# Performance work log

Hardware: AMD Instinct MI355X
Metric: run time of the kernel (lower is better)

The kernel has to match this reference:

```python
import jax, jax.numpy as jnp
import numpy as np

D_MODEL = 1024
N_EXPERTS = 8
TOP_K = 2
FFN_HIDDEN = 4 * D_MODEL


def setup_inputs() -> dict:
    key = jax.random.key(0)
    ks = jax.random.split(key, 6)
    # xavier-uniform-ish scales
    def xavier(k, shape):
        fan_in, fan_out = shape[-2], shape[-1]
        lim = jnp.sqrt(6.0 / (fan_in + fan_out))
        return jax.random.uniform(k, shape, jnp.float32, -lim, lim)
    x = jax.random.normal(ks[0], (4, 2048, D_MODEL), jnp.float32)
    w_gate = xavier(ks[1], (N_EXPERTS, D_MODEL))
    W1 = xavier(ks[2], (N_EXPERTS, D_MODEL, FFN_HIDDEN))
    b1 = jnp.zeros((N_EXPERTS, FFN_HIDDEN), jnp.float32)
    W2 = xavier(ks[3], (N_EXPERTS, FFN_HIDDEN, D_MODEL))
    b2 = jnp.zeros((N_EXPERTS, D_MODEL), jnp.float32)
    return {"x": x, "w_gate": w_gate, "W1": W1, "b1": b1, "W2": W2, "b2": b2}


def reference(x, w_gate, W1, b1, W2, b2):
    B, S, D = x.shape
    flat_x = x.reshape(-1, D)  # [T, D]
    gate = jax.nn.softmax(flat_x @ w_gate.T, axis=-1)  # [T, E]
    topk_scores, topk_idx = jax.lax.top_k(gate, TOP_K)  # [T, K]
    # combine weights per (token, expert); topk indices are distinct per token
    cw = (jax.nn.one_hot(topk_idx, N_EXPERTS, dtype=flat_x.dtype)
          * topk_scores[..., None]).sum(axis=1)  # [T, E]
    # all-expert FFN (dense grouped GEMM), then weighted combine
    h = jax.nn.gelu(jnp.einsum('td,edh->teh', flat_x, W1) + b1, approximate=False)
    y = jnp.einsum('teh,ehd->ted', h, W2) + b2  # [T, E, D]
    out = jnp.einsum('ted,te->td', y, cw)
    return out.reshape(B, S, D)
```

## Files before the change

kernel.cpp:

```cpp
#include <hip/hip_runtime.h>
#include <hip/hip_bf16.h>
#include <math.h>

#define TTOK 8192
#define DM   1024
#define NE   8
#define FH   4096
#define ECAP 8192

typedef __attribute__((ext_vector_type(8))) short bf16x8;
typedef __attribute__((ext_vector_type(4))) float f32x4;

__device__ __forceinline__ unsigned short f2bf(float f) {
  union { float f; unsigned u; } v; v.f = f;
  unsigned r = v.u + 0x7fffu + ((v.u >> 16) & 1u);
  return (unsigned short)(r >> 16);
}

__device__ __forceinline__ void async16(const unsigned short* g, unsigned short* l) {
  __builtin_amdgcn_global_load_lds(
      (const __attribute__((address_space(1))) void*)g,
      (__attribute__((address_space(3))) void*)l, 16, 0, 0);
}

__device__ __forceinline__ float gelu_erf(float v) {
  float x = v * 0.70710678118654752f;
  float ax = fabsf(x);
  float t = __frcp_rn(1.0f + 0.3275911f * ax);
  float poly = t * (0.254829592f + t * (-0.284496736f +
               t * (1.421413741f + t * (-1.453152027f + t * 1.061405429f))));
  float erfa = 1.0f - poly * __expf(-ax * ax);
  float erfx = copysignf(erfa, x);
  return 0.5f * v * (1.0f + erfx);
}

__global__ void cvt_x(const float* __restrict__ x, unsigned short* __restrict__ xb, int n4) {
  int id = blockIdx.x * 256 + threadIdx.x;
  if (id >= n4) return;
  float4 v = ((const float4*)x)[id];
  ushort4 o;
  o.x = f2bf(v.x); o.y = f2bf(v.y); o.z = f2bf(v.z); o.w = f2bf(v.w);
  ((ushort4*)xb)[id] = o;
}

__global__ __launch_bounds__(256) void transpose_cvt(
    const float* __restrict__ src, unsigned short* __restrict__ dst, int R, int Cc) {
  __shared__ unsigned short t[64 * 72];
  int e = blockIdx.z;
  int c0 = blockIdx.x * 64, r0 = blockIdx.y * 64;
  int tid = threadIdx.x;
  const float* sp = src + (size_t)e * R * Cc;
  unsigned short* dp = dst + (size_t)e * R * Cc;
#pragma unroll
  for (int p = 0; p < 4; ++p) {
    int idx = p * 256 + tid;
    int row = idx >> 4;
    int c4 = (idx & 15) * 4;
    float4 v = *(const float4*)(sp + (size_t)(r0 + row) * Cc + c0 + c4);
    t[(c4 + 0) * 72 + row] = f2bf(v.x);
    t[(c4 + 1) * 72 + row] = f2bf(v.y);
    t[(c4 + 2) * 72 + row] = f2bf(v.z);
    t[(c4 + 3) * 72 + row] = f2bf(v.w);
  }
  __syncthreads();
#pragma unroll
  for (int p = 0; p < 4; ++p) {
    int idx = p * 256 + tid;
    int crow = idx >> 4;
    int r4 = (idx & 15) * 4;
    ushort4 o = *(ushort4*)(&t[crow * 72 + r4]);
    *(ushort4*)(dp + (size_t)(c0 + crow) * R + r0 + r4) = o;
  }
}

__global__ __launch_bounds__(256) void gate_kernel(
    const float* __restrict__ x, const float* __restrict__ wg,
    int* __restrict__ cnt, int* __restrict__ ent_tok, float* __restrict__ ent_w) {
  __shared__ float wls[NE * DM];
  int tid = threadIdx.x;
  for (int i = tid; i < NE * DM / 4; i += 256)
    ((float4*)wls)[i] = ((const float4*)wg)[i];
  __syncthreads();

  int wave = tid >> 6, lane = tid & 63;
  int t = blockIdx.x * 4 + wave;
  const float* xp = x + (size_t)t * DM;
  float acc[NE];
#pragma unroll
  for (int e = 0; e < NE; ++e) acc[e] = 0.f;
#pragma unroll
  for (int i = 0; i < 16; ++i) {
    float xv = xp[i * 64 + lane];
#pragma unroll
    for (int e = 0; e < NE; ++e) acc[e] += xv * wls[e * DM + i * 64 + lane];
  }
#pragma unroll
  for (int e = 0; e < NE; ++e) {
    float v = acc[e];
    for (int off = 32; off; off >>= 1) v += __shfl_xor(v, off, 64);
    acc[e] = v;
  }
  if (lane == 0) {
    float mx = acc[0];
#pragma unroll
    for (int e = 1; e < NE; ++e) mx = fmaxf(mx, acc[e]);
    float p[NE], s = 0.f;
#pragma unroll
    for (int e = 0; e < NE; ++e) { p[e] = __expf(acc[e] - mx); s += p[e]; }
    float inv = 1.f / s;
#pragma unroll
    for (int e = 0; e < NE; ++e) p[e] *= inv;
    int i0 = 0; float m0v = p[0];
#pragma unroll
    for (int e = 1; e < NE; ++e) if (p[e] > m0v) { m0v = p[e]; i0 = e; }
    int i1 = -1; float m1v = -1.f;
#pragma unroll
    for (int e = 0; e < NE; ++e) if (e != i0 && p[e] > m1v) { m1v = p[e]; i1 = e; }
    int pos0 = atomicAdd(&cnt[i0], 1);
    ent_tok[i0 * ECAP + pos0] = t * 2;
    ent_w[i0 * ECAP + pos0] = m0v;
    int pos1 = atomicAdd(&cnt[i1], 1);
    ent_tok[i1 * ECAP + pos1] = t * 2 + 1;
    ent_w[i1 * ECAP + pos1] = m1v;
  }
}

__global__ void scan_cnt(const int* __restrict__ cnt, int* __restrict__ base) {
  if (threadIdx.x == 0) {
    int s = 0;
    for (int e = 0; e < NE; ++e) { base[e] = s; s += cnt[e]; }
  }
}

#define ISSUE_A(buf, k0)                                         \
  async16(asrc0 + (k0), &As[buf][tid * 8]);                      \
  async16(asrc1 + (k0), &As[buf][2048 + tid * 8]);

#define COMPUTE(buf)                                                           \
  {                                                                            \
    bf16x8 af[4], bfr[4];                                                      \
    _Pragma("unroll") for (int im = 0; im < 4; ++im)                           \
      af[im] = *(const bf16x8*)(&As[buf][(wm * 64 + im * 16 + l16) * 32 + q * 8]); \
    _Pragma("unroll") for (int in = 0; in < 4; ++in)                           \
      bfr[in] = *(const bf16x8*)(&Bs[buf][(wn * 64 + in * 16 + l16) * 32 + q * 8]); \
    _Pragma("unroll") for (int im = 0; im < 4; ++im)                           \
      _Pragma("unroll") for (int in = 0; in < 4; ++in)                         \
        acc[im][in] = __builtin_amdgcn_mfma_f32_16x16x32_bf16(af[im], bfr[in], acc[im][in], 0, 0, 0); \
  }

__global__ __launch_bounds__(256) void moe_gemm1(
    const unsigned short* __restrict__ xb, const unsigned short* __restrict__ W1T,
    const float* __restrict__ b1, const int* __restrict__ cnt,
    const int* __restrict__ base, const int* __restrict__ ent_tok,
    unsigned short* __restrict__ hbuf) {
  const int bid = blockIdx.x;
  const int e = bid & 7;
  const int j = bid >> 3;
  const int n0 = (j >> 6) * 128;
  const int m0 = (j & 63) * 128;
  const int C = cnt[e];
  if (m0 >= C) return;
  const int be = base[e];
  const int tid = threadIdx.x;
  const int lane = tid & 63, wave = tid >> 6;
  const int wm = wave & 1, wn = wave >> 1;
  const int q = lane >> 4, l16 = lane & 15;

  __shared__ unsigned short As[2][128 * 32];
  __shared__ unsigned short Bs[2][128 * 32];
  __shared__ float bls[128];

  if (tid < 128) bls[tid] = b1[e * FH + n0 + tid];

  const int r = tid >> 2;
  const int kq = (tid & 3) * 8;
  int i0 = m0 + r;      if (i0 >= C) i0 = C - 1;
  int i1 = m0 + r + 64; if (i1 >= C) i1 = C - 1;
  const unsigned short* asrc0 = xb + (size_t)(ent_tok[e * ECAP + i0] >> 1) * DM + kq;
  const unsigned short* asrc1 = xb + (size_t)(ent_tok[e * ECAP + i1] >> 1) * DM + kq;
  const unsigned short* bsrc  = W1T + ((size_t)e * FH + n0 + r) * DM + kq;

  f32x4 acc[4][4];
#pragma unroll
  for (int i = 0; i < 4; ++i)
#pragma unroll
    for (int jj = 0; jj < 4; ++jj) acc[i][jj] = (f32x4){0.f, 0.f, 0.f, 0.f};

  ISSUE_A(0, 0)
  async16(bsrc, &Bs[0][tid * 8]);
  async16(bsrc + (size_t)64 * DM, &Bs[0][2048 + tid * 8]);

#pragma unroll 1
  for (int k0 = 0; k0 < DM; k0 += 64) {
    __syncthreads();
    if (k0 + 32 < DM) {
      ISSUE_A(1, k0 + 32)
      async16(bsrc + k0 + 32, &Bs[1][tid * 8]);
      async16(bsrc + (size_t)64 * DM + k0 + 32, &Bs[1][2048 + tid * 8]);
    }
    COMPUTE(0)
    __syncthreads();
    if (k0 + 64 < DM) {
      ISSUE_A(0, k0 + 64)
      async16(bsrc + k0 + 64, &Bs[0][tid * 8]);
      async16(bsrc + (size_t)64 * DM + k0 + 64, &Bs[0][2048 + tid * 8]);
    }
    COMPUTE(1)
  }

#pragma unroll
  for (int im = 0; im < 4; ++im)
#pragma unroll
    for (int rr = 0; rr < 4; ++rr) {
      int gm = m0 + wm * 64 + im * 16 + q * 4 + rr;
      if (gm >= C) continue;
      size_t bas = (size_t)(be + gm) * FH;
#pragma unroll
      for (int in = 0; in < 4; ++in) {
        int n = wn * 64 + in * 16 + l16;
        float v = acc[im][in][rr] + bls[n];
        hbuf[bas + n0 + n] = f2bf(gelu_erf(v));
      }
    }
}

__global__ __launch_bounds__(256) void moe_gemm2(
    const unsigned short* __restrict__ hbuf, const unsigned short* __restrict__ W2T,
    const float* __restrict__ b2, const int* __restrict__ cnt,
    const int* __restrict__ base, const int* __restrict__ ent_tok,
    const float* __restrict__ ent_w, float* __restrict__ ybuf) {
  const int bid = blockIdx.x;
  const int e = bid & 7;
  const int j = bid >> 3;
  const int n0 = (j >> 6) * 128;
  const int m0 = (j & 63) * 128;
  const int C = cnt[e];
  if (m0 >= C) return;
  const int be = base[e];
  const int tid = threadIdx.x;
  const int lane = tid & 63, wave = tid >> 6;
  const int wm = wave & 1, wn = wave >> 1;
  const int q = lane >> 4, l16 = lane & 15;

  __shared__ unsigned short As[2][128 * 32];
  __shared__ unsigned short Bs[2][128 * 32];
  __shared__ float bls[128];

  if (tid < 128) bls[tid] = b2[e * DM + n0 + tid];

  const int r = tid >> 2;
  const int kq = (tid & 3) * 8;
  int i0 = m0 + r;      if (i0 >= C) i0 = C - 1;
  int i1 = m0 + r + 64; if (i1 >= C) i1 = C - 1;
  const unsigned short* asrc0 = hbuf + (size_t)(be + i0) * FH + kq;
  const unsigned short* asrc1 = hbuf + (size_t)(be + i1) * FH + kq;
  const unsigned short* bsrc  = W2T + ((size_t)e * DM + n0 + r) * FH + kq;

  f32x4 acc[4][4];
#pragma unroll
  for (int i = 0; i < 4; ++i)
#pragma unroll
    for (int jj = 0; jj < 4; ++jj) acc[i][jj] = (f32x4){0.f, 0.f, 0.f, 0.f};

  ISSUE_A(0, 0)
  async16(bsrc, &Bs[0][tid * 8]);
  async16(bsrc + (size_t)64 * FH, &Bs[0][2048 + tid * 8]);

#pragma unroll 1
  for (int k0 = 0; k0 < FH; k0 += 64) {
    __syncthreads();
    if (k0 + 32 < FH) {
      ISSUE_A(1, k0 + 32)
      async16(bsrc + k0 + 32, &Bs[1][tid * 8]);
      async16(bsrc + (size_t)64 * FH + k0 + 32, &Bs[1][2048 + tid * 8]);
    }
    COMPUTE(0)
    __syncthreads();
    if (k0 + 64 < FH) {
      ISSUE_A(0, k0 + 64)
      async16(bsrc + k0 + 64, &Bs[0][tid * 8]);
      async16(bsrc + (size_t)64 * FH + k0 + 64, &Bs[0][2048 + tid * 8]);
    }
    COMPUTE(1)
  }

#pragma unroll
  for (int im = 0; im < 4; ++im)
#pragma unroll
    for (int rr = 0; rr < 4; ++rr) {
      int gm = m0 + wm * 64 + im * 16 + q * 4 + rr;
      if (gm >= C) continue;
      int rowid = ent_tok[e * ECAP + gm];
      float w = ent_w[e * ECAP + gm];
      size_t bas = (size_t)rowid * DM;
#pragma unroll
      for (int in = 0; in < 4; ++in) {
        int n = wn * 64 + in * 16 + l16;
        ybuf[bas + n0 + n] = w * (acc[im][in][rr] + bls[n]);
      }
    }
}

__global__ void combine_k(const float* __restrict__ y, float* __restrict__ out, int n4) {
  int id = blockIdx.x * 256 + threadIdx.x;
  if (id >= n4) return;
  int t = id >> 8;
  int c = id & 255;
  float4 a = ((const float4*)y)[((size_t)t * 2) * 256 + c];
  float4 b = ((const float4*)y)[((size_t)t * 2 + 1) * 256 + c];
  float4 o = {a.x + b.x, a.y + b.y, a.z + b.z, a.w + b.w};
  ((float4*)out)[id] = o;
}

extern "C" void kernel_launch(void* const* d_in, const int* in_sizes, int n_in,
                              void* d_out, int out_size, void* d_ws, size_t ws_size,
                              hipStream_t stream) {
  const float* x  = (const float*)d_in[0];
  const float* wg = (const float*)d_in[1];
  const float* W1 = (const float*)d_in[2];
  const float* b1 = (const float*)d_in[3];
  const float* W2 = (const float*)d_in[4];
  const float* b2 = (const float*)d_in[5];
  float* out = (float*)d_out;

  char* ws = (char*)d_ws;
  size_t off = 0;
  unsigned short* xb = (unsigned short*)(ws + off); off += (size_t)TTOK * DM * 2;
  int* cnt = (int*)(ws + off); off += 128;
  int* base = (int*)(ws + off); off += 128;
  int* ent_tok = (int*)(ws + off); off += (size_t)NE * ECAP * 4;
  float* ent_w = (float*)(ws + off); off += (size_t)NE * ECAP * 4;
  unsigned short* W1T = (unsigned short*)(ws + off); off += (size_t)NE * DM * FH * 2;
  unsigned short* W2T = (unsigned short*)(ws + off); off += (size_t)NE * FH * DM * 2;
  unsigned short* hbuf = (unsigned short*)(ws + off); off += (size_t)TTOK * 2 * FH * 2;
  float* ybuf = (float*)W1T;

  hipMemsetAsync(cnt, 0, 128, stream);
  cvt_x<<<TTOK * DM / 4 / 256, 256, 0, stream>>>(x, xb, TTOK * DM / 4);
  gate_kernel<<<TTOK / 4, 256, 0, stream>>>(x, wg, cnt, ent_tok, ent_w);
  scan_cnt<<<1, 64, 0, stream>>>(cnt, base);
  dim3 t1(FH / 64, DM / 64, NE);
  transpose_cvt<<<t1, 256, 0, stream>>>(W1, W1T, DM, FH);
  dim3 t2(DM / 64, FH / 64, NE);
  transpose_cvt<<<t2, 256, 0, stream>>>(W2, W2T, FH, DM);
  moe_gemm1<<<16384, 256, 0, stream>>>(xb, W1T, b1, cnt, base, ent_tok, hbuf);
  moe_gemm2<<<4096, 256, 0, stream>>>(hbuf, W2T, b2, cnt, base, ent_tok, ent_w, ybuf);
  combine_k<<<TTOK * DM / 4 / 256, 256, 0, stream>>>(ybuf, out, TTOK * DM / 4);
}
```

Before: 1.027 ms.

## Replace MoE grouped GEMMs with 256x256 tile, 8-wave, swizzled LDS pipelined kernel

```diff
diff --git a/kernel.cpp b/kernel.cpp
--- a/kernel.cpp
+++ b/kernel.cpp
@@ -132,171 +132,162 @@
   }
 }
 
-#define ISSUE_A(buf, k0)                                         \
-  async16(asrc0 + (k0), &As[buf][tid * 8]);                      \
-  async16(asrc1 + (k0), &As[buf][2048 + tid * 8]);
-
-#define COMPUTE(buf)                                                           \
-  {                                                                            \
-    bf16x8 af[4], bfr[4];                                                      \
-    _Pragma("unroll") for (int im = 0; im < 4; ++im)                           \
-      af[im] = *(const bf16x8*)(&As[buf][(wm * 64 + im * 16 + l16) * 32 + q * 8]); \
-    _Pragma("unroll") for (int in = 0; in < 4; ++in)                           \
-      bfr[in] = *(const bf16x8*)(&Bs[buf][(wn * 64 + in * 16 + l16) * 32 + q * 8]); \
-    _Pragma("unroll") for (int im = 0; im < 4; ++im)                           \
-      _Pragma("unroll") for (int in = 0; in < 4; ++in)                         \
-        acc[im][in] = __builtin_amdgcn_mfma_f32_16x16x32_bf16(af[im], bfr[in], acc[im][in], 0, 0, 0); \
-  }
-
-__global__ __launch_bounds__(256) void moe_gemm1(
-    const unsigned short* __restrict__ xb, const unsigned short* __restrict__ W1T,
-    const float* __restrict__ b1, const int* __restrict__ cnt,
+
+#define LDS_BAR __builtin_amdgcn_s_barrier()
+#define WAITLGKM asm volatile("s_waitcnt lgkmcnt(0)" ::: "memory")
+#define WAITVM4  asm volatile("s_waitcnt vmcnt(4)" ::: "memory")
+#define WAITVM0  asm volatile("s_waitcnt vmcnt(0)" ::: "memory")
+
+#define LD_A8(imb)                                                                \
+  _Pragma("unroll") for (int ii = 0; ii < 4; ++ii) {                              \
+    af[ii][0] = *(const bf16x8*)(aBase + ((imb) + ii) * 2048 + rowbA + colb0);    \
+    af[ii][1] = *(const bf16x8*)(aBase + ((imb) + ii) * 2048 + rowbA + colb1);    \
+  }
+
+#define LD_B4(inb)                                                                \
+  _Pragma("unroll") for (int jj = 0; jj < 2; ++jj) {                              \
+    bf[(inb) + jj][0] = *(const bf16x8*)(bBase + ((inb) + jj) * 2048 + rowbB + colb0); \
+    bf[(inb) + jj][1] = *(const bf16x8*)(bBase + ((inb) + jj) * 2048 + rowbB + colb1); \
+  }
+
+#define MMAQ(imb, inb)                                                            \
+  _Pragma("unroll") for (int ii = 0; ii < 4; ++ii)                                \
+  _Pragma("unroll") for (int jj = 0; jj < 2; ++jj) {                              \
+    acc[(imb) + ii][(inb) + jj] = __builtin_amdgcn_mfma_f32_16x16x32_bf16(        \
+        af[ii][0], bf[(inb) + jj][0], acc[(imb) + ii][(inb) + jj], 0, 0, 0);      \
+    acc[(imb) + ii][(inb) + jj] = __builtin_amdgcn_mfma_f32_16x16x32_bf16(        \
+        af[ii][1], bf[(inb) + jj][1], acc[(imb) + ii][(inb) + jj], 0, 0, 0);      \
+  }
+
+#define STG_A(b, h, k0) {                                                         \
+    async16(pA[(h) * 2 + 0] + (k0), &sA[(b)][(h)][tid * 8]);                      \
+    async16(pA[(h) * 2 + 1] + (k0), &sA[(b)][(h)][4096 + tid * 8]);               \
+  }
+#define STG_B(b, h, k0) {                                                         \
+    async16(pB[(h) * 2 + 0] + (k0), &sB[(b)][(h)][tid * 8]);                      \
+    async16(pB[(h) * 2 + 1] + (k0), &sB[(b)][(h)][4096 + tid * 8]);               \
+  }
+
+template <int KTOT, int NTOT, bool GELU>
+__global__ __launch_bounds__(512, 2) void moe_gemm8(
+    const unsigned short* __restrict__ Asrc, const unsigned short* __restrict__ Bsrc,
+    const float* __restrict__ bias, const int* __restrict__ cnt,
     const int* __restrict__ base, const int* __restrict__ ent_tok,
-    unsigned short* __restrict__ hbuf) {
+    const float* __restrict__ ent_w, unsigned short* __restrict__ hout,
+    float* __restrict__ yout) {
   const int bid = blockIdx.x;
   const int e = bid & 7;
   const int j = bid >> 3;
-  const int n0 = (j >> 6) * 128;
-  const int m0 = (j & 63) * 128;
+  const int mt = j & 31;
+  const int nt = j >> 5;
   const int C = cnt[e];
+  const int m0 = mt * 256;
   if (m0 >= C) return;
+  const int n0 = nt * 256;
   const int be = base[e];
   const int tid = threadIdx.x;
   const int lane = tid & 63, wave = tid >> 6;
-  const int wm = wave & 1, wn = wave >> 1;
+  const int wm = wave >> 2;
+  const int wn = wave & 3;
   const int q = lane >> 4, l16 = lane & 15;
 
-  __shared__ unsigned short As[2][128 * 32];
-  __shared__ unsigned short Bs[2][128 * 32];
-  __shared__ float bls[128];
-
-  if (tid < 128) bls[tid] = b1[e * FH + n0 + tid];
-
-  const int r = tid >> 2;
-  const int kq = (tid & 3) * 8;
-  int i0 = m0 + r;      if (i0 >= C) i0 = C - 1;
-  int i1 = m0 + r + 64; if (i1 >= C) i1 = C - 1;
-  const unsigned short* asrc0 = xb + (size_t)(ent_tok[e * ECAP + i0] >> 1) * DM + kq;
-  const unsigned short* asrc1 = xb + (size_t)(ent_tok[e * ECAP + i1] >> 1) * DM + kq;
-  const unsigned short* bsrc  = W1T + ((size_t)e * FH + n0 + r) * DM + kq;
-
-  f32x4 acc[4][4];
-#pragma unroll
-  for (int i = 0; i < 4; ++i)
+  __shared__ unsigned short sA[2][2][8192];
+  __shared__ unsigned short sB[2][2][8192];
+
+  const int xorc = (((tid & 7) ^ ((tid >> 3) & 7)) << 3);
+  const unsigned short* pA[4];
+  const unsigned short* pB[4];
+#pragma unroll
+  for (int h = 0; h < 2; ++h)
+#pragma unroll
+    for (int l = 0; l < 2; ++l) {
+      const int R = h * 128 + l * 64 + (tid >> 3);
+      int i = m0 + R; if (i >= C) i = C - 1;
+      size_t arow;
+      if (GELU) arow = (size_t)(ent_tok[e * ECAP + i] >> 1);
+      else      arow = (size_t)(be + i);
+      pA[h * 2 + l] = Asrc + arow * (size_t)KTOT + xorc;
+      pB[h * 2 + l] = Bsrc + ((size_t)e * NTOT + n0 + R) * (size_t)KTOT + xorc;
+    }
+
+  const int rowbA = l16 * 128;
+  const int rowbB = ((wn & 1) * 64 + l16) * 128;
+  const int colb0 = (q * 16) ^ ((l16 & 7) << 4);
+  const int colb1 = colb0 ^ 64;
+
+  f32x4 acc[8][4];
+#pragma unroll
+  for (int i = 0; i < 8; ++i)
 #pragma unroll
     for (int jj = 0; jj < 4; ++jj) acc[i][jj] = (f32x4){0.f, 0.f, 0.f, 0.f};
-
-  ISSUE_A(0, 0)
-  async16(bsrc, &Bs[0][tid * 8]);
-  async16(bsrc + (size_t)64 * DM, &Bs[0][2048 + tid * 8]);
-
+  bf16x8 af[4][2], bf[4][2];
+
+  STG_A(0, 0, 0) STG_A(0, 1, 0)
+  STG_B(0, 0, 0) STG_B(0, 1, 0)
+  STG_B(1, 0, 64) STG_B(1, 1, 64)
+  WAITVM4;
+  LDS_BAR;
+
+  constexpr int NT = KTOT / 64;
 #pragma unroll 1
-  for (int k0 = 0; k0 < DM; k0 += 64) {
-    __syncthreads();
-    if (k0 + 32 < DM) {
-      ISSUE_A(1, k0 + 32)
-      async16(bsrc + k0 + 32, &Bs[1][tid * 8]);
-      async16(bsrc + (size_t)64 * DM + k0 + 32, &Bs[1][2048 + tid * 8]);
-    }
-    COMPUTE(0)
-    __syncthreads();
-    if (k0 + 64 < DM) {
-      ISSUE_A(0, k0 + 64)
-      async16(bsrc + k0 + 64, &Bs[0][tid * 8]);
-      async16(bsrc + (size_t)64 * DM + k0 + 64, &Bs[0][2048 + tid * 8]);
-    }
-    COMPUTE(1)
-  }
-
-#pragma unroll
-  for (int im = 0; im < 4; ++im)
+  for (int t = 0; t < NT; ++t) {
+    const int buf = t & 1;
+    const char* aBase = (const char*)&sA[buf][wm][0];
+    const char* bBase = (const char*)&sB[buf][wn >> 1][0];
+    const int kA = (t + 1) * 64;
+    const int kB = (t + 2) * 64;
+
+    LD_A8(0) LD_B4(0)
+    if (t + 1 < NT) { STG_A(buf ^ 1, 0, kA) }
+    LDS_BAR; WAITLGKM;
+    __builtin_amdgcn_s_setprio(1); MMAQ(0, 0) __builtin_amdgcn_s_setprio(0);
+    LDS_BAR;
+
+    LD_B4(2)
+    if (t + 1 < NT) { STG_A(buf ^ 1, 1, kA) }
+    LDS_BAR; WAITLGKM;
+    __builtin_amdgcn_s_setprio(1); MMAQ(0, 2) __builtin_amdgcn_s_setprio(0);
+    LDS_BAR;
+
+    LD_A8(4)
+    if (t + 2 < NT) { STG_B(buf, 0, kB) }
+    LDS_BAR; WAITLGKM;
+    __builtin_amdgcn_s_setprio(1); MMAQ(4, 0) __builtin_amdgcn_s_setprio(0);
+    LDS_BAR;
+
+    if (t + 2 < NT) { STG_B(buf, 1, kB) }
+    __builtin_amdgcn_s_setprio(1); MMAQ(4, 2) __builtin_amdgcn_s_setprio(0);
+    if (t + 2 < NT) { WAITVM4; } else { WAITVM0; }
+    LDS_BAR;
+  }
+
+  float bl[4];
+#pragma unroll
+  for (int in2 = 0; in2 < 4; ++in2)
+    bl[in2] = bias[(size_t)e * NTOT + n0 + wn * 64 + in2 * 16 + l16];
+
+#pragma unroll
+  for (int im = 0; im < 8; ++im)
 #pragma unroll
     for (int rr = 0; rr < 4; ++rr) {
-      int gm = m0 + wm * 64 + im * 16 + q * 4 + rr;
+      const int gm = m0 + wm * 128 + im * 16 + q * 4 + rr;
       if (gm >= C) continue;
-      size_t bas = (size_t)(be + gm) * FH;
-#pragma unroll
-      for (int in = 0; in < 4; ++in) {
-        int n = wn * 64 + in * 16 + l16;
-        float v = acc[im][in][rr] + bls[n];
-        hbuf[bas + n0 + n] = f2bf(gelu_erf(v));
-      }
-    }
-}
-
-__global__ __launch_bounds__(256) void moe_gemm2(
-    const unsigned short* __restrict__ hbuf, const unsigned short* __restrict__ W2T,
-    const float* __restrict__ b2, const int* __restrict__ cnt,
-    const int* __restrict__ base, const int* __restrict__ ent_tok,
-    const float* __restrict__ ent_w, float* __restrict__ ybuf) {
-  const int bid = blockIdx.x;
-  const int e = bid & 7;
-  const int j = bid >> 3;
-  const int n0 = (j >> 6) * 128;
-  const int m0 = (j & 63) * 128;
-  const int C = cnt[e];
-  if (m0 >= C) return;
-  const int be = base[e];
-  const int tid = threadIdx.x;
-  const int lane = tid & 63, wave = tid >> 6;
-  const int wm = wave & 1, wn = wave >> 1;
-  const int q = lane >> 4, l16 = lane & 15;
-
-  __shared__ unsigned short As[2][128 * 32];
-  __shared__ unsigned short Bs[2][128 * 32];
-  __shared__ float bls[128];
-
-  if (tid < 128) bls[tid] = b2[e * DM + n0 + tid];
-
-  const int r = tid >> 2;
-  const int kq = (tid & 3) * 8;
-  int i0 = m0 + r;      if (i0 >= C) i0 = C - 1;
-  int i1 = m0 + r + 64; if (i1 >= C) i1 = C - 1;
-  const unsigned short* asrc0 = hbuf + (size_t)(be + i0) * FH + kq;
-  const unsigned short* asrc1 = hbuf + (size_t)(be + i1) * FH + kq;
-  const unsigned short* bsrc  = W2T + ((size_t)e * DM + n0 + r) * FH + kq;
-
-  f32x4 acc[4][4];
-#pragma unroll
-  for (int i = 0; i < 4; ++i)
-#pragma unroll
-    for (int jj = 0; jj < 4; ++jj) acc[i][jj] = (f32x4){0.f, 0.f, 0.f, 0.f};
-
-  ISSUE_A(0, 0)
-  async16(bsrc, &Bs[0][tid * 8]);
-  async16(bsrc + (size_t)64 * FH, &Bs[0][2048 + tid * 8]);
-
-#pragma unroll 1
-  for (int k0 = 0; k0 < FH; k0 += 64) {
-    __syncthreads();
-    if (k0 + 32 < FH) {
-      ISSUE_A(1, k0 + 32)
-      async16(bsrc + k0 + 32, &Bs[1][tid * 8]);
-      async16(bsrc + (size_t)64 * FH + k0 + 32, &Bs[1][2048 + tid * 8]);
-    }
-    COMPUTE(0)
-    __syncthreads();
-    if (k0 + 64 < FH) {
-      ISSUE_A(0, k0 + 64)
-      async16(bsrc + k0 + 64, &Bs[0][tid * 8]);
-      async16(bsrc + (size_t)64 * FH + k0 + 64, &Bs[0][2048 + tid * 8]);
-    }
-    COMPUTE(1)
-  }
-
-#pragma unroll
-  for (int im = 0; im < 4; ++im)
-#pragma unroll
-    for (int rr = 0; rr < 4; ++rr) {
-      int gm = m0 + wm * 64 + im * 16 + q * 4 + rr;
-      if (gm >= C) continue;
-      int rowid = ent_tok[e * ECAP + gm];
-      float w = ent_w[e * ECAP + gm];
-      size_t bas = (size_t)rowid * DM;
-#pragma unroll
-      for (int in = 0; in < 4; ++in) {
-        int n = wn * 64 + in * 16 + l16;
-        ybuf[bas + n0 + n] = w * (acc[im][in][rr] + bls[n]);
+      if (GELU) {
+        const size_t bas = (size_t)(be + gm) * NTOT + n0;
+#pragma unroll
+        for (int in2 = 0; in2 < 4; ++in2) {
+          const int n = wn * 64 + in2 * 16 + l16;
+          hout[bas + n] = f2bf(gelu_erf(acc[im][in2][rr] + bl[in2]));
+        }
+      } else {
+        const int rowid = ent_tok[e * ECAP + gm];
+        const float w = ent_w[e * ECAP + gm];
+        const size_t bas = (size_t)rowid * NTOT + n0;
+#pragma unroll
+        for (int in2 = 0; in2 < 4; ++in2) {
+          const int n = wn * 64 + in2 * 16 + l16;
+          yout[bas + n] = w * (acc[im][in2][rr] + bl[in2]);
+        }
       }
     }
 }
@@ -343,7 +334,9 @@
   transpose_cvt<<<t1, 256, 0, stream>>>(W1, W1T, DM, FH);
   dim3 t2(DM / 64, FH / 64, NE);
   transpose_cvt<<<t2, 256, 0, stream>>>(W2, W2T, FH, DM);
-  moe_gemm1<<<16384, 256, 0, stream>>>(xb, W1T, b1, cnt, base, ent_tok, hbuf);
-  moe_gemm2<<<4096, 256, 0, stream>>>(hbuf, W2T, b2, cnt, base, ent_tok, ent_w, ybuf);
+  moe_gemm8<DM, FH, true><<<NE * 32 * (FH / 256), 512, 0, stream>>>(
+      xb, W1T, b1, cnt, base, ent_tok, ent_w, hbuf, nullptr);
+  moe_gemm8<FH, DM, false><<<NE * 32 * (DM / 256), 512, 0, stream>>>(
+      hbuf, W2T, b2, cnt, base, ent_tok, ent_w, nullptr, ybuf);
   combine_k<<<TTOK * DM / 4 / 256, 256, 0, stream>>>(ybuf, out, TTOK * DM / 4);
 }
```

Result: slower. 1.076 ms (+4.8%).
